# Kernel optimization log

Measured on AMD Instinct MI355X. Metric: run time of the kernel, lower is better.

Reference implementation:

```python
import jax, jax.numpy as jnp
import numpy as np

N_NODES = 10000
NEG_SLOPE_ATT = 0.5   # GATConv negative_slope
NEG_SLOPE_ACT = 0.01  # F.leaky_relu default used as self.act


def setup_inputs() -> dict:
    key = jax.random.key(0)
    k1, k2, k3, k4, k5 = jax.random.split(key, 5)
    in_dim, out_dim = 512, 128
    x = jax.random.normal(k1, (N_NODES, in_dim), dtype=jnp.float32)
    edge_index = jax.random.randint(k2, (2, 320000), 0, N_NODES, dtype=jnp.int64)
    # glorot-ish scaled params
    W = jax.random.normal(k3, (in_dim, out_dim), dtype=jnp.float32) * (1.0 / np.sqrt(in_dim))
    att_src = jax.random.normal(k4, (out_dim,), dtype=jnp.float32) * (1.0 / np.sqrt(out_dim))
    att_dst = jax.random.normal(k5, (out_dim,), dtype=jnp.float32) * (1.0 / np.sqrt(out_dim))
    bias = jnp.zeros((out_dim,), dtype=jnp.float32)
    return {"x": x, "edge_index": edge_index, "W": W,
            "att_src": att_src, "att_dst": att_dst, "bias": bias}


def _leaky(v, slope):
    return jnp.where(v >= 0, v, slope * v)


def reference(x, edge_index, W, att_src, att_dst, bias):
    N = x.shape[0]
    loop = jnp.arange(N, dtype=edge_index.dtype)
    src = jnp.concatenate([edge_index[0], loop])  # message source j
    dst = jnp.concatenate([edge_index[1], loop])  # message target i

    h = x @ W                      # [N, out_dim]
    a_src = h @ att_src            # [N]
    a_dst = h @ att_dst            # [N]

    e = _leaky(a_src[src] + a_dst[dst], NEG_SLOPE_ATT)   # [E+N]
    # segment softmax over incoming edges of each dst node
    m = jax.ops.segment_max(e, dst, num_segments=N)
    ex = jnp.exp(e - m[dst])
    denom = jax.ops.segment_sum(ex, dst, num_segments=N)
    alpha = ex / denom[dst]

    out = jax.ops.segment_sum(h[src] * alpha[:, None], dst, num_segments=N) + bias
    embed_x = _leaky(out, NEG_SLOPE_ACT)                 # self.act = F.leaky_relu
    recon = jax.nn.sigmoid(embed_x @ embed_x.T)          # [N, N]
    return recon, embed_x
```

## Files before the change

### kernel.cpp

```cpp
#include <hip/hip_runtime.h>
#include <stdint.h>


typedef __attribute__((ext_vector_type(8))) short short8v;
typedef __attribute__((ext_vector_type(4))) float f32x4;

#define IN_DIM 512
#define OUT_DIM 128
#define NEG_ATT 0.5f
#define NEG_ACT 0.01f

__device__ __forceinline__ float leakyf(float v, float s) { return v >= 0.f ? v : s * v; }

__device__ __forceinline__ uint16_t f2bf(float v) {
  uint32_t u = __float_as_uint(v);
  u += 0x7FFFu + ((u >> 16) & 1u);
  return (uint16_t)(u >> 16);
}

__global__ __launch_bounds__(256) void k_h_gemm(const float* __restrict__ x,
                                                const float* __restrict__ W,
                                                const float* __restrict__ att_s_g,
                                                const float* __restrict__ att_d_g,
                                                float* __restrict__ h,
                                                float* __restrict__ a_src,
                                                float* __restrict__ a_dst, int N) {
  int tid = threadIdx.x;
  int tx = tid & 31, ty = tid >> 5;
  int row0 = blockIdx.x * 32 + ty * 4;
  int rc[4];
  #pragma unroll
  for (int r = 0; r < 4; ++r) rc[r] = (row0 + r < N) ? (row0 + r) : (N - 1);

  f32x4 acc[4];
  #pragma unroll
  for (int r = 0; r < 4; ++r) acc[r] = (f32x4){0.f, 0.f, 0.f, 0.f};

  for (int k = 0; k < IN_DIM; k += 4) {
    f32x4 wreg[4];
    #pragma unroll
    for (int kk = 0; kk < 4; ++kk)
      wreg[kk] = *(const f32x4*)&W[(size_t)(k + kk) * OUT_DIM + tx * 4];
    #pragma unroll
    for (int r = 0; r < 4; ++r) {
      f32x4 xv = *(const f32x4*)&x[(size_t)rc[r] * IN_DIM + k];
      #pragma unroll
      for (int kk = 0; kk < 4; ++kk) {
        acc[r][0] = fmaf(xv[kk], wreg[kk][0], acc[r][0]);
        acc[r][1] = fmaf(xv[kk], wreg[kk][1], acc[r][1]);
        acc[r][2] = fmaf(xv[kk], wreg[kk][2], acc[r][2]);
        acc[r][3] = fmaf(xv[kk], wreg[kk][3], acc[r][3]);
      }
    }
  }

  float atts[4], attd[4];
  #pragma unroll
  for (int j = 0; j < 4; ++j) { atts[j] = att_s_g[tx * 4 + j]; attd[j] = att_d_g[tx * 4 + j]; }
  #pragma unroll
  for (int r = 0; r < 4; ++r) {
    int row = row0 + r;
    float ps = 0.f, pd = 0.f;
    #pragma unroll
    for (int j = 0; j < 4; ++j) { ps = fmaf(acc[r][j], atts[j], ps); pd = fmaf(acc[r][j], attd[j], pd); }
    #pragma unroll
    for (int off = 16; off; off >>= 1) {
      ps += __shfl_xor(ps, off);
      pd += __shfl_xor(pd, off);
    }
    if (row < N) {
      *(f32x4*)&h[(size_t)row * OUT_DIM + tx * 4] = acc[r];
      if (tx == 0) { a_src[row] = ps; a_dst[row] = pd; }
    }
  }
}

__global__ void k_zero(int* __restrict__ p, int n) {
  int i = blockIdx.x * blockDim.x + threadIdx.x;
  if (i < n) p[i] = 0;
}
__global__ void k_count(const int* __restrict__ dst, int* __restrict__ cnt, int E) {
  int e = blockIdx.x * blockDim.x + threadIdx.x;
  if (e < E) atomicAdd(&cnt[dst[e]], 1);
}
__global__ __launch_bounds__(1024) void k_scan(const int* __restrict__ cnt,
                                               int* __restrict__ row_start, int N) {
  __shared__ int sd[1024];
  int t = threadIdx.x;
  const int CH = (N + 1023) >> 10;
  int base = t * CH;
  int s = 0;
  for (int k = 0; k < CH; ++k) { int i = base + k; if (i < N) s += cnt[i]; }
  sd[t] = s;
  __syncthreads();
  for (int off = 1; off < 1024; off <<= 1) {
    int v = (t >= off) ? sd[t - off] : 0;
    __syncthreads();
    sd[t] += v;
    __syncthreads();
  }
  int run = (t == 0) ? 0 : sd[t - 1];
  for (int k = 0; k < CH; ++k) {
    int i = base + k;
    if (i < N) { row_start[i] = run; run += cnt[i]; }
  }
  if (t == 1023) row_start[N] = sd[1023];
}
__global__ void k_copy(const int* __restrict__ a, int* __restrict__ b, int n) {
  int i = blockIdx.x * blockDim.x + threadIdx.x;
  if (i < n) b[i] = a[i];
}
__global__ void k_fill(const int* __restrict__ src, const int* __restrict__ dst,
                       int* __restrict__ cursor, int* __restrict__ csr, int E) {
  int e = blockIdx.x * blockDim.x + threadIdx.x;
  if (e < E) {
    int d = dst[e];
    int pos = atomicAdd(&cursor[d], 1);
    csr[pos] = src[e];
  }
}

__global__ void k_pad(uint16_t* __restrict__ ebf, int N, int NPAD) {
  int total = (NPAD - N) * OUT_DIM;
  for (int i = threadIdx.x + blockIdx.x * blockDim.x; i < total; i += blockDim.x * gridDim.x)
    ebf[(size_t)N * OUT_DIM + i] = 0;
}

__global__ __launch_bounds__(256) void k_aggregate(
    const float* __restrict__ h, const float* __restrict__ a_src,
    const float* __restrict__ a_dst, const int* __restrict__ row_start,
    const int* __restrict__ csr, const float* __restrict__ bias,
    float* __restrict__ embed_out, uint16_t* __restrict__ ebf, int N) {
  int wid = (int)((blockIdx.x * blockDim.x + threadIdx.x) >> 6);
  int lane = threadIdx.x & 63;
  if (wid >= N) return;
  int i = wid;
  int s0 = row_start[i], s1 = row_start[i + 1];
  float adst = a_dst[i];
  float eself = leakyf(a_src[i] + adst, NEG_ATT);
  float m = eself;
  for (int k = s0 + lane; k < s1; k += 64) {
    float e = leakyf(a_src[csr[k]] + adst, NEG_ATT);
    m = fmaxf(m, e);
  }
  #pragma unroll
  for (int off = 32; off; off >>= 1) m = fmaxf(m, __shfl_xor(m, off));
  float dsum = 0.f;
  for (int k = s0 + lane; k < s1; k += 64) {
    float e = leakyf(a_src[csr[k]] + adst, NEG_ATT);
    dsum += __expf(e - m);
  }
  #pragma unroll
  for (int off = 32; off; off >>= 1) dsum += __shfl_xor(dsum, off);
  dsum += __expf(eself - m);
  float inv = 1.0f / dsum;
  float wself = __expf(eself - m) * inv;
  float acc0 = h[(size_t)i * OUT_DIM + lane] * wself;
  float acc1 = h[(size_t)i * OUT_DIM + 64 + lane] * wself;
  #pragma unroll 4
  for (int k = s0; k < s1; ++k) {
    int s = csr[k];
    float w = __expf(leakyf(a_src[s] + adst, NEG_ATT) - m) * inv;
    acc0 = fmaf(h[(size_t)s * OUT_DIM + lane], w, acc0);
    acc1 = fmaf(h[(size_t)s * OUT_DIM + 64 + lane], w, acc1);
  }
  float o0 = leakyf(acc0 + bias[lane], NEG_ACT);
  float o1 = leakyf(acc1 + bias[64 + lane], NEG_ACT);
  embed_out[(size_t)i * OUT_DIM + lane] = o0;
  embed_out[(size_t)i * OUT_DIM + 64 + lane] = o1;
  ebf[(size_t)i * OUT_DIM + lane] = f2bf(o0);
  ebf[(size_t)i * OUT_DIM + 64 + lane] = f2bf(o1);
}

__global__ __launch_bounds__(512, 4) void k_recon(const uint16_t* __restrict__ ebf,
                                                  float* __restrict__ out,
                                                  int N, int nb) {
  __shared__ __align__(16) unsigned char smem[66560];
  uint16_t* sA = (uint16_t*)smem;
  uint16_t* sB = (uint16_t*)(smem + 32768);
  float* sO = (float*)smem;

  int tid = threadIdx.x;
  int wid = tid >> 6, lane = tid & 63;
  int wr = wid >> 2, wc = wid & 3;
  int r16 = lane & 15, kg = lane >> 4;

  int nwg = nb * nb;
  int q = nwg >> 3, r8 = nwg & 7;
  int orig = blockIdx.x;
  int xcd = orig & 7, sub = orig >> 3;
  int swz = (xcd < r8 ? xcd * (q + 1) : r8 * (q + 1) + (xcd - r8) * q) + sub;
  int by = swz / nb, bx = swz - by * nb;
  int rowBlk = by * 128, colBlk = bx * 128;

  #pragma unroll
  for (int p = 0; p < 4; ++p) {
    int i2 = p * 512 + tid;
    int row = i2 >> 4, slot = i2 & 15;
    f32x4 va = *(const f32x4*)&ebf[(size_t)(rowBlk + row) * OUT_DIM + slot * 8];
    f32x4 vb = *(const f32x4*)&ebf[(size_t)(colBlk + row) * OUT_DIM + slot * 8];
    int ss = slot ^ (row & 7);
    *(f32x4*)&sA[row * OUT_DIM + ss * 8] = va;
    *(f32x4*)&sB[row * OUT_DIM + ss * 8] = vb;
  }
  __syncthreads();

  int rowWl = wr * 64, colWl = wc * 32;
  f32x4 acc[4][2];
  #pragma unroll
  for (int a = 0; a < 4; ++a)
    #pragma unroll
    for (int b = 0; b < 2; ++b) acc[a][b] = (f32x4){0.f, 0.f, 0.f, 0.f};

  #pragma unroll
  for (int kc = 0; kc < 4; ++kc) {
    short8v bfr[2];
    #pragma unroll
    for (int tj = 0; tj < 2; ++tj) {
      int rw = colWl + tj * 16 + r16;
      int ss = (kc * 4 + kg) ^ (rw & 7);
      bfr[tj] = *(const short8v*)&sB[rw * OUT_DIM + ss * 8];
    }
    #pragma unroll
    for (int ti = 0; ti < 4; ++ti) {
      int rw = rowWl + ti * 16 + r16;
      int ss = (kc * 4 + kg) ^ (rw & 7);
      short8v af = *(const short8v*)&sA[rw * OUT_DIM + ss * 8];
      #pragma unroll
      for (int tj = 0; tj < 2; ++tj)
        acc[ti][tj] = __builtin_amdgcn_mfma_f32_16x16x32_bf16(af, bfr[tj], acc[ti][tj], 0, 0, 0);
    }
  }

  bool colFull = (colBlk + 128 <= N);
  #pragma unroll
  for (int s = 0; s < 2; ++s) {
    __syncthreads();
    if (wr == s) {
      #pragma unroll
      for (int ti = 0; ti < 4; ++ti)
        #pragma unroll
        for (int tj = 0; tj < 2; ++tj)
          #pragma unroll
          for (int qq = 0; qq < 4; ++qq)
            sO[(ti * 16 + kg * 4 + qq) * 133 + wc * 32 + tj * 16 + r16] = acc[ti][tj][qq];
    }
    __syncthreads();
    int srow0 = rowBlk + s * 64;
    #pragma unroll
    for (int p = 0; p < 4; ++p) {
      int i2 = p * 512 + tid;
      int row = i2 >> 5, c = i2 & 31;
      f32x4 v = *(const f32x4*)&sO[row * 133 + c * 4];
      #pragma unroll
      for (int j = 0; j < 4; ++j) v[j] = 1.0f / (1.0f + __expf(-v[j]));
      int rr = srow0 + row;
      if (rr < N) {
        int col = colBlk + c * 4;
        if (colFull) {
          __builtin_nontemporal_store(v, (f32x4*)&out[(size_t)rr * N + col]);
        } else {
          #pragma unroll
          for (int j = 0; j < 4; ++j)
            if (col + j < N) __builtin_nontemporal_store(v[j], &out[(size_t)rr * N + col + j]);
        }
      }
    }
  }
}

extern "C" void kernel_launch(void* const* d_in, const int* in_sizes, int n_in,
                              void* d_out, int out_size, void* d_ws, size_t ws_size,
                              hipStream_t stream) {
  const float* x = (const float*)d_in[0];
  const int* ei = (const int*)d_in[1];
  const float* W = (const float*)d_in[2];
  const float* att_s = (const float*)d_in[3];
  const float* att_d = (const float*)d_in[4];
  const float* bias = (const float*)d_in[5];

  const int N = in_sizes[0] / IN_DIM;
  const int E = in_sizes[1] / 2;
  const int NB = (N + 127) / 128;
  const int NPAD = NB * 128;

  float* out = (float*)d_out;
  float* embed_out = out + (size_t)N * N;

  float* h = (float*)d_ws;
  float* a_src = h + (size_t)N * OUT_DIM;
  float* a_dst = a_src + N;
  int* cnt = (int*)(a_dst + N);
  int* row_start = cnt + N;
  int* cursor = row_start + (N + 4);
  int* csr = cursor + N;
  uint16_t* ebf = (uint16_t*)(csr + E);

  const int* e_src = ei;
  const int* e_dst = ei + E;

  k_h_gemm<<<dim3((N + 31) / 32), 256, 0, stream>>>(x, W, att_s, att_d, h, a_src, a_dst, N);
  k_zero<<<dim3((N + 255) / 256), 256, 0, stream>>>(cnt, N);
  k_count<<<dim3((E + 255) / 256), 256, 0, stream>>>(e_dst, cnt, E);
  k_scan<<<dim3(1), 1024, 0, stream>>>(cnt, row_start, N);
  k_copy<<<dim3((N + 255) / 256), 256, 0, stream>>>(row_start, cursor, N);
  k_fill<<<dim3((E + 255) / 256), 256, 0, stream>>>(e_src, e_dst, cursor, csr, E);
  k_pad<<<dim3(8), 256, 0, stream>>>(ebf, N, NPAD);
  k_aggregate<<<dim3((N * 64 + 255) / 256), 256, 0, stream>>>(
      h, a_src, a_dst, row_start, csr, bias, embed_out, ebf, N);
  k_recon<<<dim3(NB * NB), 512, 0, stream>>>(ebf, out, N, NB);
}
```

Before: 247.7 us.

## Fuse edge counting, cursor copy and padding into neighbouring kernels

Moves the dst-degree atomic counting into the h GEMM kernel, halving its row tile so the grid covers all edges. The scan now writes the cursor array directly, padding rows are zeroed by extra aggregate waves, and the zero kernel becomes a memset. This removes several small kernel launches at the cost of a less register-efficient GEMM tile. The fused count covers only blockIdx*512 edges, so correctness depends on E fitting the grid.

```diff
diff --git a/kernel.cpp b/kernel.cpp
--- a/kernel.cpp
+++ b/kernel.cpp
@@ -22,19 +22,21 @@
                                                 const float* __restrict__ W,
                                                 const float* __restrict__ att_s_g,
                                                 const float* __restrict__ att_d_g,
+                                                const int* __restrict__ e_dst,
+                                                int* __restrict__ cnt, int E,
                                                 float* __restrict__ h,
                                                 float* __restrict__ a_src,
                                                 float* __restrict__ a_dst, int N) {
   int tid = threadIdx.x;
   int tx = tid & 31, ty = tid >> 5;
-  int row0 = blockIdx.x * 32 + ty * 4;
-  int rc[4];
-  #pragma unroll
-  for (int r = 0; r < 4; ++r) rc[r] = (row0 + r < N) ? (row0 + r) : (N - 1);
-
-  f32x4 acc[4];
-  #pragma unroll
-  for (int r = 0; r < 4; ++r) acc[r] = (f32x4){0.f, 0.f, 0.f, 0.f};
+  int row0 = blockIdx.x * 16 + ty * 2;
+  int rc[2];
+  #pragma unroll
+  for (int r = 0; r < 2; ++r) rc[r] = (row0 + r < N) ? (row0 + r) : (N - 1);
+
+  f32x4 acc[2];
+  #pragma unroll
+  for (int r = 0; r < 2; ++r) acc[r] = (f32x4){0.f, 0.f, 0.f, 0.f};
 
   for (int k = 0; k < IN_DIM; k += 4) {
     f32x4 wreg[4];
@@ -42,7 +44,7 @@
     for (int kk = 0; kk < 4; ++kk)
       wreg[kk] = *(const f32x4*)&W[(size_t)(k + kk) * OUT_DIM + tx * 4];
     #pragma unroll
-    for (int r = 0; r < 4; ++r) {
+    for (int r = 0; r < 2; ++r) {
       f32x4 xv = *(const f32x4*)&x[(size_t)rc[r] * IN_DIM + k];
       #pragma unroll
       for (int kk = 0; kk < 4; ++kk) {
@@ -58,7 +60,7 @@
   #pragma unroll
   for (int j = 0; j < 4; ++j) { atts[j] = att_s_g[tx * 4 + j]; attd[j] = att_d_g[tx * 4 + j]; }
   #pragma unroll
-  for (int r = 0; r < 4; ++r) {
+  for (int r = 0; r < 2; ++r) {
     int row = row0 + r;
     float ps = 0.f, pd = 0.f;
     #pragma unroll
@@ -73,18 +75,16 @@
       if (tx == 0) { a_src[row] = ps; a_dst[row] = pd; }
     }
   }
-}
-
-__global__ void k_zero(int* __restrict__ p, int n) {
-  int i = blockIdx.x * blockDim.x + threadIdx.x;
-  if (i < n) p[i] = 0;
-}
-__global__ void k_count(const int* __restrict__ dst, int* __restrict__ cnt, int E) {
-  int e = blockIdx.x * blockDim.x + threadIdx.x;
-  if (e < E) atomicAdd(&cnt[dst[e]], 1);
-}
+
+  int e0 = blockIdx.x * 512 + tid;
+  if (e0 < E) atomicAdd(&cnt[e_dst[e0]], 1);
+  int e1 = e0 + 256;
+  if (e1 < E) atomicAdd(&cnt[e_dst[e1]], 1);
+}
+
 __global__ __launch_bounds__(1024) void k_scan(const int* __restrict__ cnt,
-                                               int* __restrict__ row_start, int N) {
+                                               int* __restrict__ row_start,
+                                               int* __restrict__ cursor, int N) {
   __shared__ int sd[1024];
   int t = threadIdx.x;
   const int CH = (N + 1023) >> 10;
@@ -102,13 +102,9 @@
   int run = (t == 0) ? 0 : sd[t - 1];
   for (int k = 0; k < CH; ++k) {
     int i = base + k;
-    if (i < N) { row_start[i] = run; run += cnt[i]; }
+    if (i < N) { row_start[i] = run; cursor[i] = run; run += cnt[i]; }
   }
   if (t == 1023) row_start[N] = sd[1023];
-}
-__global__ void k_copy(const int* __restrict__ a, int* __restrict__ b, int n) {
-  int i = blockIdx.x * blockDim.x + threadIdx.x;
-  if (i < n) b[i] = a[i];
 }
 __global__ void k_fill(const int* __restrict__ src, const int* __restrict__ dst,
                        int* __restrict__ cursor, int* __restrict__ csr, int E) {
@@ -120,20 +116,20 @@
   }
 }
 
-__global__ void k_pad(uint16_t* __restrict__ ebf, int N, int NPAD) {
-  int total = (NPAD - N) * OUT_DIM;
-  for (int i = threadIdx.x + blockIdx.x * blockDim.x; i < total; i += blockDim.x * gridDim.x)
-    ebf[(size_t)N * OUT_DIM + i] = 0;
-}
-
 __global__ __launch_bounds__(256) void k_aggregate(
     const float* __restrict__ h, const float* __restrict__ a_src,
     const float* __restrict__ a_dst, const int* __restrict__ row_start,
     const int* __restrict__ csr, const float* __restrict__ bias,
-    float* __restrict__ embed_out, uint16_t* __restrict__ ebf, int N) {
+    float* __restrict__ embed_out, uint16_t* __restrict__ ebf, int N, int NPAD) {
   int wid = (int)((blockIdx.x * blockDim.x + threadIdx.x) >> 6);
   int lane = threadIdx.x & 63;
-  if (wid >= N) return;
+  if (wid >= N) {
+    if (wid < NPAD) {
+      ebf[(size_t)wid * OUT_DIM + lane] = 0;
+      ebf[(size_t)wid * OUT_DIM + 64 + lane] = 0;
+    }
+    return;
+  }
   int i = wid;
   int s0 = row_start[i], s1 = row_start[i + 1];
   float adst = a_dst[i];
@@ -299,14 +295,12 @@
   const int* e_src = ei;
   const int* e_dst = ei + E;
 
-  k_h_gemm<<<dim3((N + 31) / 32), 256, 0, stream>>>(x, W, att_s, att_d, h, a_src, a_dst, N);
-  k_zero<<<dim3((N + 255) / 256), 256, 0, stream>>>(cnt, N);
-  k_count<<<dim3((E + 255) / 256), 256, 0, stream>>>(e_dst, cnt, E);
-  k_scan<<<dim3(1), 1024, 0, stream>>>(cnt, row_start, N);
-  k_copy<<<dim3((N + 255) / 256), 256, 0, stream>>>(row_start, cursor, N);
+  hipMemsetAsync(cnt, 0, (size_t)N * sizeof(int), stream);
+  k_h_gemm<<<dim3((N + 15) / 16), 256, 0, stream>>>(x, W, att_s, att_d,
+                                                    e_dst, cnt, E, h, a_src, a_dst, N);
+  k_scan<<<dim3(1), 1024, 0, stream>>>(cnt, row_start, cursor, N);
   k_fill<<<dim3((E + 255) / 256), 256, 0, stream>>>(e_src, e_dst, cursor, csr, E);
-  k_pad<<<dim3(8), 256, 0, stream>>>(ebf, N, NPAD);
-  k_aggregate<<<dim3((N * 64 + 255) / 256), 256, 0, stream>>>(
-      h, a_src, a_dst, row_start, csr, bias, embed_out, ebf, N);
+  k_aggregate<<<dim3((NPAD * 64 + 255) / 256), 256, 0, stream>>>(
+      h, a_src, a_dst, row_start, csr, bias, embed_out, ebf, N, NPAD);
   k_recon<<<dim3(NB * NB), 512, 0, stream>>>(ebf, out, N, NB);
 }
```

Result: faster. 232.6 us (-6.1%).
